# Kernel optimization log

Measured on AMD Instinct MI355X. Metric: run time of the kernel, lower is better.

The kernel has to match this reference:

```python
import jax, jax.numpy as jnp
import numpy as np

N_NODES = 50000
N_EDGES = 800000
IN_CH = 128
HID = 128
OUT_CH = 12
NUM_GRAPHS = 512


def _gcn_layer(x, src, dst, W, b, n):
    # GCNConv: out = D^{-1/2} (A + I) D^{-1/2} (x W) + b, messages flow src -> dst
    h = x @ W
    loops = jnp.arange(n)
    s = jnp.concatenate([src, loops])
    d = jnp.concatenate([dst, loops])
    deg = jax.ops.segment_sum(jnp.ones(s.shape[0], dtype=h.dtype), d, num_segments=n)
    dinv = jnp.where(deg > 0, jax.lax.rsqrt(deg), 0.0)
    norm = dinv[s] * dinv[d]                      # [E+N]
    msg = h[s] * norm[:, None]                    # gather + scale
    out = jax.ops.segment_sum(msg, d, num_segments=n)  # scatter-add to targets
    return out + b


def setup_inputs() -> dict:
    key = jax.random.key(0)
    ks = jax.random.split(key, 12)
    x = jax.random.normal(ks[0], (N_NODES, IN_CH), dtype=jnp.float32)
    edge_index = jax.random.randint(ks[1], (2, N_EDGES), 0, N_NODES, dtype=jnp.int64)
    batch = jnp.sort(jax.random.randint(ks[2], (N_NODES,), 0, NUM_GRAPHS, dtype=jnp.int64))
    sc = 0.05
    W0 = jax.random.normal(ks[3], (IN_CH, HID), dtype=jnp.float32) * sc
    b0 = jnp.zeros((HID,), dtype=jnp.float32)
    W1 = jax.random.normal(ks[4], (HID, HID), dtype=jnp.float32) * sc
    b1 = jnp.zeros((HID,), dtype=jnp.float32)
    W2 = jax.random.normal(ks[5], (HID, HID), dtype=jnp.float32) * sc
    b2 = jnp.zeros((HID,), dtype=jnp.float32)
    Wc = jax.random.normal(ks[6], (HID, OUT_CH), dtype=jnp.float32) * sc
    bc = jnp.zeros((OUT_CH,), dtype=jnp.float32)
    return {"x": x, "edge_index": edge_index, "batch": batch,
            "W0": W0, "b0": b0, "W1": W1, "b1": b1, "W2": W2, "b2": b2,
            "Wc": Wc, "bc": bc}


def reference(x, edge_index, batch, W0, b0, W1, b1, W2, b2, Wc, bc):
    src, dst = edge_index[0], edge_index[1]
    n = x.shape[0]
    h = _gcn_layer(x, src, dst, W0, b0, n)
    h = jax.nn.relu(h)  # dropout is identity in eval mode
    h = _gcn_layer(h, src, dst, W1, b1, n)
    h = jax.nn.relu(h)
    h = _gcn_layer(h, src, dst, W2, b2, n)
    # global_mean_pool by graph id
    sums = jax.ops.segment_sum(h, batch, num_segments=NUM_GRAPHS)
    cnt = jax.ops.segment_sum(jnp.ones((n,), dtype=h.dtype), batch, num_segments=NUM_GRAPHS)
    pooled = sums / jnp.maximum(cnt, 1.0)[:, None]
    return pooled @ Wc + bc
```

## Files before the change

### kernel.cpp

```cpp
#include <hip/hip_runtime.h>
#include <hip/hip_bf16.h>


#define CH  128
#define CAP 64
#define NW  8

typedef unsigned int  uint;
typedef unsigned short ushort;
typedef __attribute__((ext_vector_type(8))) short  short8;
typedef __attribute__((ext_vector_type(4))) float  f32x4;
typedef __attribute__((ext_vector_type(4))) int    i32x4;

__device__ inline float bflo(uint u) { return __uint_as_float(u << 16); }
__device__ inline float bfhi(uint u) { return __uint_as_float(u & 0xffff0000u); }
__device__ inline ushort f2bf(float f) {
    uint u = __float_as_uint(f);
    return (ushort)((u + 0x7fffu + ((u >> 16) & 1u)) >> 16);
}

__global__ __launch_bounds__(256) void k_prep0(int4* __restrict__ len4, int nz,
                                               const int* __restrict__ batch,
                                               int* __restrict__ gstart, int n, int G,
                                               const float* __restrict__ W0,
                                               const float* __restrict__ W1,
                                               const float* __restrict__ W2,
                                               ushort* __restrict__ Wt0,
                                               ushort* __restrict__ Wt1,
                                               ushort* __restrict__ Wt2,
                                               int ZB, int BB) {
    int b = blockIdx.x;
    int t = threadIdx.x;
    if (b < ZB) {
        int i = b * 256 + t;
        if (i < nz) len4[i] = make_int4(0, 0, 0, 0);
    } else if (b < ZB + BB) {
        int v = (b - ZB) * 256 + t;
        if (v <= n) {
            int prev = (v == 0) ? -1 : batch[v - 1];
            int cur  = (v == n) ? G  : batch[v];
            for (int g = prev + 1; g <= cur; ++g) gstart[g] = v;
        }
    } else {
        int m = b - ZB - BB;
        const float* W = (m == 0) ? W0 : (m == 1) ? W1 : W2;
        ushort* Wt = (m == 0) ? Wt0 : (m == 1) ? Wt1 : Wt2;
        const float4* wsrc = (const float4*)W;
        #pragma unroll
        for (int i = 0; i < 16; ++i) {
            int c4 = t + i * 256;
            int k  = c4 >> 5;
            int n0 = (c4 & 31) * 4;
            float4 v = wsrc[c4];
            Wt[(n0 + 0) * CH + k] = f2bf(v.x);
            Wt[(n0 + 1) * CH + k] = f2bf(v.y);
            Wt[(n0 + 2) * CH + k] = f2bf(v.z);
            Wt[(n0 + 3) * CH + k] = f2bf(v.w);
        }
    }
}

__global__ __launch_bounds__(256) void k_scatter(const int* __restrict__ src,
                                                 const int* __restrict__ dstv,
                                                 int* __restrict__ len,
                                                 ushort* __restrict__ csr_src,
                                                 int E, int nper) {
    int p = blockIdx.x & (NW - 1);
    int chunk = blockIdx.x >> 3;
    int lo = p * nper, hi = lo + nper;
    int e0 = (chunk * 256 + threadIdx.x) * 4;
    if (e0 + 3 < E) {
        i32x4 d4 = __builtin_nontemporal_load((const i32x4*)&dstv[e0]);
        #pragma unroll
        for (int j = 0; j < 4; ++j) {
            int d = d4[j];
            if (d >= lo && d < hi) {
                int pos = atomicAdd(&len[d], 1);
                if (pos < CAP) csr_src[d * CAP + pos] = (ushort)src[e0 + j];
            }
        }
    } else {
        for (int e = e0; e < E; ++e) {
            int d = dstv[e];
            if (d >= lo && d < hi) {
                int pos = atomicAdd(&len[d], 1);
                if (pos < CAP) csr_src[d * CAP + pos] = (ushort)src[e];
            }
        }
    }
}

__global__ __launch_bounds__(256) void k_dinv(const int* __restrict__ len,
                                              float* __restrict__ dinv, int n) {
    int v = blockIdx.x * 256 + threadIdx.x;
    if (v < n) dinv[v] = 1.0f / sqrtf((float)(len[v] + 1));
}

template<int IN_BF16>
__global__ __launch_bounds__(256) void k_gemm_mfma(const void* __restrict__ Ain,
                                                   const ushort* __restrict__ Wt,
                                                   ushort* __restrict__ C, int M) {
    int tid = threadIdx.x;
    int wid = tid >> 6, lane = tid & 63;
    int row = blockIdx.x * 64 + wid * 16 + (lane & 15);
    int lk  = (lane >> 4) * 8;
    bool rok = row < M;
    f32x4 acc[8] = {};
    #pragma unroll
    for (int ks = 0; ks < 4; ++ks) {
        short8 af = {};
        if (rok) {
            if (IN_BF16) {
                af = *(const short8*)&((const ushort*)Ain)[(size_t)row * CH + ks * 32 + lk];
            } else {
                const float* Af = (const float*)Ain;
                float4 a0 = *(const float4*)&Af[(size_t)row * CH + ks * 32 + lk];
                float4 a1 = *(const float4*)&Af[(size_t)row * CH + ks * 32 + lk + 4];
                af[0] = (short)f2bf(a0.x); af[1] = (short)f2bf(a0.y);
                af[2] = (short)f2bf(a0.z); af[3] = (short)f2bf(a0.w);
                af[4] = (short)f2bf(a1.x); af[5] = (short)f2bf(a1.y);
                af[6] = (short)f2bf(a1.z); af[7] = (short)f2bf(a1.w);
            }
        }
        #pragma unroll
        for (int nt = 0; nt < 8; ++nt) {
            short8 bf = *(const short8*)&Wt[(size_t)(nt * 16 + (lane & 15)) * CH + ks * 32 + lk];
            acc[nt] = __builtin_amdgcn_mfma_f32_16x16x32_bf16(af, bf, acc[nt], 0, 0, 0);
        }
    }
    int ci = (lane >> 4) * 4;
    int cj = lane & 15;
    int rb = blockIdx.x * 64 + wid * 16 + ci;
    #pragma unroll
    for (int nt = 0; nt < 8; ++nt) {
        #pragma unroll
        for (int r = 0; r < 4; ++r) {
            int grow = rb + r;
            if (grow < M) C[(size_t)grow * CH + nt * 16 + cj] = f2bf(acc[nt][r]);
        }
    }
}

template<int OB>
__global__ __launch_bounds__(256) void k_agg(const ushort* __restrict__ T,
                                             const int* __restrict__ len,
                                             const ushort* __restrict__ csr,
                                             const float* __restrict__ dinv,
                                             const float* __restrict__ bias,
                                             void* __restrict__ outv,
                                             int n, int do_relu) {
    int wid = threadIdx.x >> 6;
    int lane = threadIdx.x & 63;
    int v = blockIdx.x * 4 + wid;
    if (v >= n) return;
    int q = lane >> 4;
    int l16 = lane & 15;
    int c = l16 * 8;
    float acc[8] = {};
    int end = min(len[v], CAP);
    const ushort* row_csr = csr + (size_t)v * CAP;
    #pragma unroll 2
    for (int p = q; p < end; p += 4) {
        int s = row_csr[p];
        float w = dinv[s];
        uint4 row = *(const uint4*)&T[(size_t)s * CH + c];
        acc[0] += w * bflo(row.x); acc[1] += w * bfhi(row.x);
        acc[2] += w * bflo(row.y); acc[3] += w * bfhi(row.y);
        acc[4] += w * bflo(row.z); acc[5] += w * bfhi(row.z);
        acc[6] += w * bflo(row.w); acc[7] += w * bfhi(row.w);
    }
    #pragma unroll
    for (int j = 0; j < 8; ++j) {
        acc[j] += __shfl_xor(acc[j], 16, 64);
        acc[j] += __shfl_xor(acc[j], 32, 64);
    }
    if (q == 0) {
        float di = dinv[v];
        uint4 sv = *(const uint4*)&T[(size_t)v * CH + c];
        float s0 = bflo(sv.x), s1 = bfhi(sv.x), s2 = bflo(sv.y), s3 = bfhi(sv.y);
        float s4 = bflo(sv.z), s5 = bfhi(sv.z), s6 = bflo(sv.w), s7 = bfhi(sv.w);
        float4 ba = *(const float4*)&bias[c];
        float4 bb = *(const float4*)&bias[c + 4];
        float o[8];
        o[0] = (acc[0] + di * s0) * di + ba.x;
        o[1] = (acc[1] + di * s1) * di + ba.y;
        o[2] = (acc[2] + di * s2) * di + ba.z;
        o[3] = (acc[3] + di * s3) * di + ba.w;
        o[4] = (acc[4] + di * s4) * di + bb.x;
        o[5] = (acc[5] + di * s5) * di + bb.y;
        o[6] = (acc[6] + di * s6) * di + bb.z;
        o[7] = (acc[7] + di * s7) * di + bb.w;
        if (do_relu) {
            #pragma unroll
            for (int j = 0; j < 8; ++j) o[j] = fmaxf(o[j], 0.f);
        }
        if (OB) {
            ushort u[8];
            #pragma unroll
            for (int j = 0; j < 8; ++j) u[j] = f2bf(o[j]);
            *(short8*)&((ushort*)outv)[(size_t)v * CH + c] = *(short8*)u;
        } else {
            float* out = (float*)outv;
            *(float4*)&out[(size_t)v * CH + c]     = make_float4(o[0], o[1], o[2], o[3]);
            *(float4*)&out[(size_t)v * CH + c + 4] = make_float4(o[4], o[5], o[6], o[7]);
        }
    }
}

__global__ __launch_bounds__(128) void k_poolcls(const float* __restrict__ h,
                                                 const int* __restrict__ gstart,
                                                 const float* __restrict__ Wc,
                                                 const float* __restrict__ bc,
                                                 float* __restrict__ out, int OUT) {
    __shared__ float p[CH];
    int g = blockIdx.x;
    int t = threadIdx.x;
    int beg = gstart[g], end = gstart[g + 1];
    float acc = 0.f;
    for (int v = beg; v < end; ++v) acc += h[(size_t)v * CH + t];
    float cnt = fmaxf((float)(end - beg), 1.0f);
    p[t] = acc / cnt;
    __syncthreads();
    if (t < OUT) {
        float s = bc[t];
        for (int k = 0; k < CH; ++k) s += p[k] * Wc[k * OUT + t];
        out[g * OUT + t] = s;
    }
}

extern "C" void kernel_launch(void* const* d_in, const int* in_sizes, int n_in,
                              void* d_out, int out_size, void* d_ws, size_t ws_size,
                              hipStream_t stream) {
    const float* x     = (const float*)d_in[0];
    const int*   eidx  = (const int*)d_in[1];
    const int*   batch = (const int*)d_in[2];
    const float* W0 = (const float*)d_in[3];
    const float* b0 = (const float*)d_in[4];
    const float* W1 = (const float*)d_in[5];
    const float* b1 = (const float*)d_in[6];
    const float* W2 = (const float*)d_in[7];
    const float* b2 = (const float*)d_in[8];
    const float* Wc = (const float*)d_in[9];
    const float* bc = (const float*)d_in[10];
    float* out = (float*)d_out;

    const int n = in_sizes[0] / CH;
    const int E = in_sizes[1] / 2;
    const int OUT = 12;
    const int G = out_size / OUT;
    const int* src = eidx;
    const int* dst = eidx + E;

    char* ws = (char*)d_ws;
    size_t off = 0;
    auto carve = [&](size_t bytes) -> char* {
        off = (off + 255) & ~(size_t)255;
        char* p = ws + off;
        off += bytes;
        return p;
    };
    int*    len     = (int*)carve((size_t)n * 4);
    float*  dinv    = (float*)carve((size_t)n * 4);
    int*    gstart  = (int*)carve((size_t)(G + 1) * 4);
    ushort* Wt0     = (ushort*)carve((size_t)CH * CH * 2);
    ushort* Wt1     = (ushort*)carve((size_t)CH * CH * 2);
    ushort* Wt2     = (ushort*)carve((size_t)CH * CH * 2);
    ushort* csr_src = (ushort*)carve((size_t)n * CAP * 2);
    ushort* T       = (ushort*)carve((size_t)n * CH * 2);
    ushort* bufA    = (ushort*)carve((size_t)n * CH * 2);
    ushort* bufB    = (ushort*)carve((size_t)n * CH * 2);
    float*  bufF    = (float*)carve((size_t)n * CH * 4);
    (void)ws_size;

    const int GB = (n + 63) / 64;
    const int agg_grid = (n + 3) / 4;
    const int nper = (n + NW - 1) / NW;
    const int chunks = (E + 1023) / 1024;
    const int ZB = (n / 4 + 255) / 256;
    const int BB = (n + 1 + 255) / 256;

    k_prep0<<<ZB + BB + 3, 256, 0, stream>>>((int4*)len, n / 4, batch, gstart,
                                             n, G, W0, W1, W2, Wt0, Wt1, Wt2,
                                             ZB, BB);
    k_scatter<<<chunks * NW, 256, 0, stream>>>(src, dst, len, csr_src, E, nper);
    k_dinv<<<(n + 255) / 256, 256, 0, stream>>>(len, dinv, n);

    k_gemm_mfma<0><<<GB, 256, 0, stream>>>(x, Wt0, T, n);
    k_agg<1><<<agg_grid, 256, 0, stream>>>(T, len, csr_src, dinv, b0, bufA, n, 1);
    k_gemm_mfma<1><<<GB, 256, 0, stream>>>(bufA, Wt1, T, n);
    k_agg<1><<<agg_grid, 256, 0, stream>>>(T, len, csr_src, dinv, b1, bufB, n, 1);
    k_gemm_mfma<1><<<GB, 256, 0, stream>>>(bufB, Wt2, T, n);
    k_agg<0><<<agg_grid, 256, 0, stream>>>(T, len, csr_src, dinv, b2, bufF, n, 0);

    k_poolcls<<<G, CH, 0, stream>>>(bufF, gstart, Wc, bc, out, OUT);
}
```

Before: 263.1 us.

## Fuse aggregation with next-layer GEMM and final aggregation with mean pooling

Each aggregation now builds a 64-node tile of post-ReLU bf16 features in shared memory and multiplies it directly by the next layer's weights with MFMA. This removes the intermediate activation buffers and the separate GEMM launches. The final aggregation sums rows into per-graph pooled totals in shared memory and atomically adds them, which replaces the sequential per-graph pooling kernel. The scatter kernel now handles 8 edges per thread, and the pool buffer is zeroed in the prep kernel. In exchange, each wave handles 16 nodes one after another, which may reduce parallelism in the latency-bound gather.

```diff
diff --git a/kernel.cpp b/kernel.cpp
--- a/kernel.cpp
+++ b/kernel.cpp
@@ -20,6 +20,7 @@
 }
 
 __global__ __launch_bounds__(256) void k_prep0(int4* __restrict__ len4, int nz,
+                                               int4* __restrict__ pool4, int npz,
                                                const int* __restrict__ batch,
                                                int* __restrict__ gstart, int n, int G,
                                                const float* __restrict__ W0,
@@ -28,21 +29,24 @@
                                                ushort* __restrict__ Wt0,
                                                ushort* __restrict__ Wt1,
                                                ushort* __restrict__ Wt2,
-                                               int ZB, int BB) {
+                                               int ZB, int PB, int BB) {
     int b = blockIdx.x;
     int t = threadIdx.x;
     if (b < ZB) {
         int i = b * 256 + t;
         if (i < nz) len4[i] = make_int4(0, 0, 0, 0);
-    } else if (b < ZB + BB) {
-        int v = (b - ZB) * 256 + t;
+    } else if (b < ZB + PB) {
+        int i = (b - ZB) * 256 + t;
+        if (i < npz) pool4[i] = make_int4(0, 0, 0, 0);
+    } else if (b < ZB + PB + BB) {
+        int v = (b - ZB - PB) * 256 + t;
         if (v <= n) {
             int prev = (v == 0) ? -1 : batch[v - 1];
             int cur  = (v == n) ? G  : batch[v];
             for (int g = prev + 1; g <= cur; ++g) gstart[g] = v;
         }
     } else {
-        int m = b - ZB - BB;
+        int m = b - ZB - PB - BB;
         const float* W = (m == 0) ? W0 : (m == 1) ? W1 : W2;
         ushort* Wt = (m == 0) ? Wt0 : (m == 1) ? Wt1 : Wt2;
         const float4* wsrc = (const float4*)W;
@@ -68,15 +72,24 @@
     int p = blockIdx.x & (NW - 1);
     int chunk = blockIdx.x >> 3;
     int lo = p * nper, hi = lo + nper;
-    int e0 = (chunk * 256 + threadIdx.x) * 4;
-    if (e0 + 3 < E) {
-        i32x4 d4 = __builtin_nontemporal_load((const i32x4*)&dstv[e0]);
+    int e0 = (chunk * 256 + threadIdx.x) * 8;
+    if (e0 + 7 < E) {
+        i32x4 d4a = *(const i32x4*)&dstv[e0];
+        i32x4 d4b = *(const i32x4*)&dstv[e0 + 4];
         #pragma unroll
         for (int j = 0; j < 4; ++j) {
-            int d = d4[j];
+            int d = d4a[j];
             if (d >= lo && d < hi) {
                 int pos = atomicAdd(&len[d], 1);
                 if (pos < CAP) csr_src[d * CAP + pos] = (ushort)src[e0 + j];
+            }
+        }
+        #pragma unroll
+        for (int j = 0; j < 4; ++j) {
+            int d = d4b[j];
+            if (d >= lo && d < hi) {
+                int pos = atomicAdd(&len[d], 1);
+                if (pos < CAP) csr_src[d * CAP + pos] = (ushort)src[e0 + 4 + j];
             }
         }
     } else {
@@ -96,10 +109,9 @@
     if (v < n) dinv[v] = 1.0f / sqrtf((float)(len[v] + 1));
 }
 
-template<int IN_BF16>
-__global__ __launch_bounds__(256) void k_gemm_mfma(const void* __restrict__ Ain,
-                                                   const ushort* __restrict__ Wt,
-                                                   ushort* __restrict__ C, int M) {
+__global__ __launch_bounds__(256) void k_gemm0(const float* __restrict__ Af,
+                                               const ushort* __restrict__ Wt,
+                                               ushort* __restrict__ C, int M) {
     int tid = threadIdx.x;
     int wid = tid >> 6, lane = tid & 63;
     int row = blockIdx.x * 64 + wid * 16 + (lane & 15);
@@ -110,17 +122,12 @@
     for (int ks = 0; ks < 4; ++ks) {
         short8 af = {};
         if (rok) {
-            if (IN_BF16) {
-                af = *(const short8*)&((const ushort*)Ain)[(size_t)row * CH + ks * 32 + lk];
-            } else {
-                const float* Af = (const float*)Ain;
-                float4 a0 = *(const float4*)&Af[(size_t)row * CH + ks * 32 + lk];
-                float4 a1 = *(const float4*)&Af[(size_t)row * CH + ks * 32 + lk + 4];
-                af[0] = (short)f2bf(a0.x); af[1] = (short)f2bf(a0.y);
-                af[2] = (short)f2bf(a0.z); af[3] = (short)f2bf(a0.w);
-                af[4] = (short)f2bf(a1.x); af[5] = (short)f2bf(a1.y);
-                af[6] = (short)f2bf(a1.z); af[7] = (short)f2bf(a1.w);
-            }
+            float4 a0 = *(const float4*)&Af[(size_t)row * CH + ks * 32 + lk];
+            float4 a1 = *(const float4*)&Af[(size_t)row * CH + ks * 32 + lk + 4];
+            af[0] = (short)f2bf(a0.x); af[1] = (short)f2bf(a0.y);
+            af[2] = (short)f2bf(a0.z); af[3] = (short)f2bf(a0.w);
+            af[4] = (short)f2bf(a1.x); af[5] = (short)f2bf(a1.y);
+            af[6] = (short)f2bf(a1.z); af[7] = (short)f2bf(a1.w);
         }
         #pragma unroll
         for (int nt = 0; nt < 8; ++nt) {
@@ -141,85 +148,167 @@
     }
 }
 
-template<int OB>
-__global__ __launch_bounds__(256) void k_agg(const ushort* __restrict__ T,
-                                             const int* __restrict__ len,
-                                             const ushort* __restrict__ csr,
-                                             const float* __restrict__ dinv,
-                                             const float* __restrict__ bias,
-                                             void* __restrict__ outv,
-                                             int n, int do_relu) {
-    int wid = threadIdx.x >> 6;
-    int lane = threadIdx.x & 63;
-    int v = blockIdx.x * 4 + wid;
-    if (v >= n) return;
-    int q = lane >> 4;
-    int l16 = lane & 15;
+__global__ __launch_bounds__(256) void k_agg_gemm(const ushort* __restrict__ T,
+                                                  const int* __restrict__ len,
+                                                  const ushort* __restrict__ csr,
+                                                  const float* __restrict__ dinv,
+                                                  const float* __restrict__ bias,
+                                                  const ushort* __restrict__ Wt,
+                                                  ushort* __restrict__ Tout,
+                                                  int n) {
+    __shared__ ushort hs[64][136];
+    int tid = threadIdx.x;
+    int wid = tid >> 6, lane = tid & 63;
+    int q = lane >> 4, l16 = lane & 15;
     int c = l16 * 8;
-    float acc[8] = {};
-    int end = min(len[v], CAP);
-    const ushort* row_csr = csr + (size_t)v * CAP;
-    #pragma unroll 2
-    for (int p = q; p < end; p += 4) {
-        int s = row_csr[p];
-        float w = dinv[s];
-        uint4 row = *(const uint4*)&T[(size_t)s * CH + c];
-        acc[0] += w * bflo(row.x); acc[1] += w * bfhi(row.x);
-        acc[2] += w * bflo(row.y); acc[3] += w * bfhi(row.y);
-        acc[4] += w * bflo(row.z); acc[5] += w * bfhi(row.z);
-        acc[6] += w * bflo(row.w); acc[7] += w * bfhi(row.w);
-    }
+    int base = blockIdx.x * 64;
+    for (int i = 0; i < 16; ++i) {
+        int v = base + wid * 16 + i;
+        if (v >= n) break;
+        float acc[8] = {};
+        int end = min(len[v], CAP);
+        const ushort* row_csr = csr + (size_t)v * CAP;
+        #pragma unroll 2
+        for (int p = q; p < end; p += 4) {
+            int s = row_csr[p];
+            float w = dinv[s];
+            uint4 row = *(const uint4*)&T[(size_t)s * CH + c];
+            acc[0] += w * bflo(row.x); acc[1] += w * bfhi(row.x);
+            acc[2] += w * bflo(row.y); acc[3] += w * bfhi(row.y);
+            acc[4] += w * bflo(row.z); acc[5] += w * bfhi(row.z);
+            acc[6] += w * bflo(row.w); acc[7] += w * bfhi(row.w);
+        }
+        #pragma unroll
+        for (int j = 0; j < 8; ++j) {
+            acc[j] += __shfl_xor(acc[j], 16, 64);
+            acc[j] += __shfl_xor(acc[j], 32, 64);
+        }
+        if (q == 0) {
+            float di = dinv[v];
+            uint4 sv = *(const uint4*)&T[(size_t)v * CH + c];
+            float s0 = bflo(sv.x), s1 = bfhi(sv.x), s2 = bflo(sv.y), s3 = bfhi(sv.y);
+            float s4 = bflo(sv.z), s5 = bfhi(sv.z), s6 = bflo(sv.w), s7 = bfhi(sv.w);
+            float4 ba = *(const float4*)&bias[c];
+            float4 bb = *(const float4*)&bias[c + 4];
+            ushort u[8];
+            u[0] = f2bf(fmaxf((acc[0] + di * s0) * di + ba.x, 0.f));
+            u[1] = f2bf(fmaxf((acc[1] + di * s1) * di + ba.y, 0.f));
+            u[2] = f2bf(fmaxf((acc[2] + di * s2) * di + ba.z, 0.f));
+            u[3] = f2bf(fmaxf((acc[3] + di * s3) * di + ba.w, 0.f));
+            u[4] = f2bf(fmaxf((acc[4] + di * s4) * di + bb.x, 0.f));
+            u[5] = f2bf(fmaxf((acc[5] + di * s5) * di + bb.y, 0.f));
+            u[6] = f2bf(fmaxf((acc[6] + di * s6) * di + bb.z, 0.f));
+            u[7] = f2bf(fmaxf((acc[7] + di * s7) * di + bb.w, 0.f));
+            *(short8*)&hs[wid * 16 + i][c] = *(short8*)u;
+        }
+    }
+    int row_l = wid * 16 + l16;
+    bool rok = (base + row_l) < n;
+    int lk = q * 8;
+    f32x4 acc2[8] = {};
     #pragma unroll
-    for (int j = 0; j < 8; ++j) {
-        acc[j] += __shfl_xor(acc[j], 16, 64);
-        acc[j] += __shfl_xor(acc[j], 32, 64);
-    }
-    if (q == 0) {
-        float di = dinv[v];
-        uint4 sv = *(const uint4*)&T[(size_t)v * CH + c];
-        float s0 = bflo(sv.x), s1 = bfhi(sv.x), s2 = bflo(sv.y), s3 = bfhi(sv.y);
-        float s4 = bflo(sv.z), s5 = bfhi(sv.z), s6 = bflo(sv.w), s7 = bfhi(sv.w);
-        float4 ba = *(const float4*)&bias[c];
-        float4 bb = *(const float4*)&bias[c + 4];
-        float o[8];
-        o[0] = (acc[0] + di * s0) * di + ba.x;
-        o[1] = (acc[1] + di * s1) * di + ba.y;
-        o[2] = (acc[2] + di * s2) * di + ba.z;
-        o[3] = (acc[3] + di * s3) * di + ba.w;
-        o[4] = (acc[4] + di * s4) * di + bb.x;
-        o[5] = (acc[5] + di * s5) * di + bb.y;
-        o[6] = (acc[6] + di * s6) * di + bb.z;
-        o[7] = (acc[7] + di * s7) * di + bb.w;
-        if (do_relu) {
-            #pragma unroll
-            for (int j = 0; j < 8; ++j) o[j] = fmaxf(o[j], 0.f);
-        }
-        if (OB) {
-            ushort u[8];
-            #pragma unroll
-            for (int j = 0; j < 8; ++j) u[j] = f2bf(o[j]);
-            *(short8*)&((ushort*)outv)[(size_t)v * CH + c] = *(short8*)u;
-        } else {
-            float* out = (float*)outv;
-            *(float4*)&out[(size_t)v * CH + c]     = make_float4(o[0], o[1], o[2], o[3]);
-            *(float4*)&out[(size_t)v * CH + c + 4] = make_float4(o[4], o[5], o[6], o[7]);
-        }
-    }
-}
-
-__global__ __launch_bounds__(128) void k_poolcls(const float* __restrict__ h,
-                                                 const int* __restrict__ gstart,
-                                                 const float* __restrict__ Wc,
-                                                 const float* __restrict__ bc,
-                                                 float* __restrict__ out, int OUT) {
+    for (int ks = 0; ks < 4; ++ks) {
+        short8 af = {};
+        if (rok) af = *(const short8*)&hs[row_l][ks * 32 + lk];
+        #pragma unroll
+        for (int nt = 0; nt < 8; ++nt) {
+            short8 bf = *(const short8*)&Wt[(size_t)(nt * 16 + l16) * CH + ks * 32 + lk];
+            acc2[nt] = __builtin_amdgcn_mfma_f32_16x16x32_bf16(af, bf, acc2[nt], 0, 0, 0);
+        }
+    }
+    int ci = q * 4;
+    int rb = base + wid * 16 + ci;
+    #pragma unroll
+    for (int nt = 0; nt < 8; ++nt) {
+        #pragma unroll
+        for (int r = 0; r < 4; ++r) {
+            int grow = rb + r;
+            if (grow < n) Tout[(size_t)grow * CH + nt * 16 + l16] = f2bf(acc2[nt][r]);
+        }
+    }
+}
+
+__global__ __launch_bounds__(256) void k_agg_pool(const ushort* __restrict__ T,
+                                                  const int* __restrict__ len,
+                                                  const ushort* __restrict__ csr,
+                                                  const float* __restrict__ dinv,
+                                                  const float* __restrict__ bias,
+                                                  const int* __restrict__ batch,
+                                                  float* __restrict__ pool,
+                                                  int n) {
+    __shared__ float hf[64][128];
+    __shared__ int bb[64];
+    int tid = threadIdx.x;
+    int wid = tid >> 6, lane = tid & 63;
+    int q = lane >> 4, l16 = lane & 15;
+    int c = l16 * 8;
+    int base = blockIdx.x * 64;
+    for (int i = 0; i < 16; ++i) {
+        int v = base + wid * 16 + i;
+        if (v >= n) break;
+        float acc[8] = {};
+        int end = min(len[v], CAP);
+        const ushort* row_csr = csr + (size_t)v * CAP;
+        #pragma unroll 2
+        for (int p = q; p < end; p += 4) {
+            int s = row_csr[p];
+            float w = dinv[s];
+            uint4 row = *(const uint4*)&T[(size_t)s * CH + c];
+            acc[0] += w * bflo(row.x); acc[1] += w * bfhi(row.x);
+            acc[2] += w * bflo(row.y); acc[3] += w * bfhi(row.y);
+            acc[4] += w * bflo(row.z); acc[5] += w * bfhi(row.z);
+            acc[6] += w * bflo(row.w); acc[7] += w * bfhi(row.w);
+        }
+        #pragma unroll
+        for (int j = 0; j < 8; ++j) {
+            acc[j] += __shfl_xor(acc[j], 16, 64);
+            acc[j] += __shfl_xor(acc[j], 32, 64);
+        }
+        if (q == 0) {
+            float di = dinv[v];
+            uint4 sv = *(const uint4*)&T[(size_t)v * CH + c];
+            float s0 = bflo(sv.x), s1 = bfhi(sv.x), s2 = bflo(sv.y), s3 = bfhi(sv.y);
+            float s4 = bflo(sv.z), s5 = bfhi(sv.z), s6 = bflo(sv.w), s7 = bfhi(sv.w);
+            float4 ba = *(const float4*)&bias[c];
+            float4 bb4 = *(const float4*)&bias[c + 4];
+            int lr = wid * 16 + i;
+            *(float4*)&hf[lr][c] = make_float4(
+                (acc[0] + di * s0) * di + ba.x, (acc[1] + di * s1) * di + ba.y,
+                (acc[2] + di * s2) * di + ba.z, (acc[3] + di * s3) * di + ba.w);
+            *(float4*)&hf[lr][c + 4] = make_float4(
+                (acc[4] + di * s4) * di + bb4.x, (acc[5] + di * s5) * di + bb4.y,
+                (acc[6] + di * s6) * di + bb4.z, (acc[7] + di * s7) * di + bb4.w);
+            if (l16 == 0) bb[lr] = batch[v];
+        }
+    }
+    __syncthreads();
+    int nvalid = min(64, n - base);
+    if (tid < CH && nvalid > 0) {
+        float acc = 0.f;
+        int gcur = bb[0];
+        for (int i = 0; i < nvalid; ++i) {
+            int g = bb[i];
+            if (g != gcur) {
+                atomicAdd(&pool[gcur * CH + tid], acc);
+                acc = 0.f;
+                gcur = g;
+            }
+            acc += hf[i][tid];
+        }
+        atomicAdd(&pool[gcur * CH + tid], acc);
+    }
+}
+
+__global__ __launch_bounds__(128) void k_cls(const float* __restrict__ pool,
+                                             const int* __restrict__ gstart,
+                                             const float* __restrict__ Wc,
+                                             const float* __restrict__ bc,
+                                             float* __restrict__ out, int OUT) {
     __shared__ float p[CH];
     int g = blockIdx.x;
     int t = threadIdx.x;
-    int beg = gstart[g], end = gstart[g + 1];
-    float acc = 0.f;
-    for (int v = beg; v < end; ++v) acc += h[(size_t)v * CH + t];
-    float cnt = fmaxf((float)(end - beg), 1.0f);
-    p[t] = acc / cnt;
+    float cnt = fmaxf((float)(gstart[g + 1] - gstart[g]), 1.0f);
+    p[t] = pool[g * CH + t] / cnt;
     __syncthreads();
     if (t < OUT) {
         float s = bc[t];
@@ -262,35 +351,33 @@
     int*    len     = (int*)carve((size_t)n * 4);
     float*  dinv    = (float*)carve((size_t)n * 4);
     int*    gstart  = (int*)carve((size_t)(G + 1) * 4);
+    float*  pool    = (float*)carve((size_t)G * CH * 4);
     ushort* Wt0     = (ushort*)carve((size_t)CH * CH * 2);
     ushort* Wt1     = (ushort*)carve((size_t)CH * CH * 2);
     ushort* Wt2     = (ushort*)carve((size_t)CH * CH * 2);
     ushort* csr_src = (ushort*)carve((size_t)n * CAP * 2);
-    ushort* T       = (ushort*)carve((size_t)n * CH * 2);
-    ushort* bufA    = (ushort*)carve((size_t)n * CH * 2);
-    ushort* bufB    = (ushort*)carve((size_t)n * CH * 2);
-    float*  bufF    = (float*)carve((size_t)n * CH * 4);
+    ushort* T0      = (ushort*)carve((size_t)n * CH * 2);
+    ushort* T1      = (ushort*)carve((size_t)n * CH * 2);
     (void)ws_size;
 
-    const int GB = (n + 63) / 64;
-    const int agg_grid = (n + 3) / 4;
+    const int FB = (n + 63) / 64;
     const int nper = (n + NW - 1) / NW;
-    const int chunks = (E + 1023) / 1024;
+    const int chunks = (E + 2047) / 2048;
     const int ZB = (n / 4 + 255) / 256;
+    const int PB = (G * CH / 4 + 255) / 256;
     const int BB = (n + 1 + 255) / 256;
 
-    k_prep0<<<ZB + BB + 3, 256, 0, stream>>>((int4*)len, n / 4, batch, gstart,
-                                             n, G, W0, W1, W2, Wt0, Wt1, Wt2,
-                                             ZB, BB);
+    k_prep0<<<ZB + PB + BB + 3, 256, 0, stream>>>((int4*)len, n / 4,
+                                                  (int4*)pool, G * CH / 4,
+                                                  batch, gstart, n, G,
+                                                  W0, W1, W2, Wt0, Wt1, Wt2,
+                                                  ZB, PB, BB);
     k_scatter<<<chunks * NW, 256, 0, stream>>>(src, dst, len, csr_src, E, nper);
     k_dinv<<<(n + 255) / 256, 256, 0, stream>>>(len, dinv, n);
 
-    k_gemm_mfma<0><<<GB, 256, 0, stream>>>(x, Wt0, T, n);
-    k_agg<1><<<agg_grid, 256, 0, stream>>>(T, len, csr_src, dinv, b0, bufA, n, 1);
-    k_gemm_mfma<1><<<GB, 256, 0, stream>>>(bufA, Wt1, T, n);
-    k_agg<1><<<agg_grid, 256, 0, stream>>>(T, len, csr_src, dinv, b1, bufB, n, 1);
-    k_gemm_mfma<1><<<GB, 256, 0, stream>>>(bufB, Wt2, T, n);
-    k_agg<0><<<agg_grid, 256, 0, stream>>>(T, len, csr_src, dinv, b2, bufF, n, 0);
-
-    k_poolcls<<<G, CH, 0, stream>>>(bufF, gstart, Wc, bc, out, OUT);
-}
+    k_gemm0<<<FB, 256, 0, stream>>>(x, Wt0, T0, n);
+    k_agg_gemm<<<FB, 256, 0, stream>>>(T0, len, csr_src, dinv, b0, Wt1, T1, n);
+    k_agg_gemm<<<FB, 256, 0, stream>>>(T1, len, csr_src, dinv, b1, Wt2, T0, n);
+    k_agg_pool<<<FB, 256, 0, stream>>>(T0, len, csr_src, dinv, b2, batch, pool, n);
+    k_cls<<<G, CH, 0, stream>>>(pool, gstart, Wc, bc, out, OUT);
+}
```

After: 273.8 us. 1.04x slower.
